# Kernel optimization log

Hardware: AMD Instinct MI355X
Metric: run time of the kernel (lower is better)

## Reference

```python
import jax, jax.numpy as jnp
import numpy as np
from functools import partial

N_FEATURES = 32
UNITS = [64, 32]
NUM_HEADS = 4
KEY_DIM = UNITS[-1] // NUM_HEADS  # 8
PRED_LEN = 24
B, T = 4096, 336


def _p(key, shape, scale=0.05):
    return scale * jax.random.normal(key, shape, dtype=jnp.float32)


def setup_inputs() -> dict:
    key = jax.random.key(0)
    ks = jax.random.split(key, 20)
    d = UNITS[-1]  # 32, model dim entering attention
    return {
        "x": jax.random.normal(ks[0], (B, T, N_FEATURES), dtype=jnp.float32),
        # LSTM layer 1: in=32, units=64
        "W1": _p(ks[1], (N_FEATURES, 4 * UNITS[0])),
        "U1": _p(ks[2], (UNITS[0], 4 * UNITS[0])),
        "b1": jnp.zeros((4 * UNITS[0],), jnp.float32),
        # LSTM layer 2: in=64, units=32
        "W2": _p(ks[3], (UNITS[0], 4 * UNITS[1])),
        "U2": _p(ks[4], (UNITS[1], 4 * UNITS[1])),
        "b2": jnp.zeros((4 * UNITS[1],), jnp.float32),
        # MultiHeadAttention projections (Keras layout)
        "Wq": _p(ks[5], (d, NUM_HEADS, KEY_DIM)),
        "bq": jnp.zeros((NUM_HEADS, KEY_DIM), jnp.float32),
        "Wk": _p(ks[6], (d, NUM_HEADS, KEY_DIM)),
        "bk": jnp.zeros((NUM_HEADS, KEY_DIM), jnp.float32),
        "Wv": _p(ks[7], (d, NUM_HEADS, KEY_DIM)),
        "bv": jnp.zeros((NUM_HEADS, KEY_DIM), jnp.float32),
        "Wo": _p(ks[8], (NUM_HEADS, KEY_DIM, d)),
        "bo": jnp.zeros((d,), jnp.float32),
        # Dense head
        "Wd1": _p(ks[9], (d, 64)),
        "bd1": jnp.zeros((64,), jnp.float32),
        "Wd2": _p(ks[10], (64, PRED_LEN)),
        "bd2": jnp.zeros((PRED_LEN,), jnp.float32),
    }


def _lstm(x, W, U, b, return_sequences):
    # x: [B, T, in]; Keras gate order: i, f, c(candidate), o
    Bb = x.shape[0]
    u = U.shape[0]
    x_t = jnp.swapaxes(x, 0, 1)  # [T, B, in]
    xz = x_t @ W + b             # precompute input contribution: [T, B, 4u]

    def step(carry, zx):
        h, c = carry
        z = zx + h @ U
        i, f, g, o = jnp.split(z, 4, axis=-1)
        i = jax.nn.sigmoid(i)
        f = jax.nn.sigmoid(f)
        g = jnp.tanh(g)
        o = jax.nn.sigmoid(o)
        c = f * c + i * g
        h = o * jnp.tanh(c)
        return (h, c), h

    init = (jnp.zeros((Bb, u), x.dtype), jnp.zeros((Bb, u), x.dtype))
    (h_last, _), hs = jax.lax.scan(step, init, xz)
    return jnp.swapaxes(hs, 0, 1) if return_sequences else h_last


def _mha_seq1(x, Wq, bq, Wk, bk, Wv, bv, Wo, bo):
    # x: [B, d]; attention over a seq-len-1 axis (faithful to tf.expand_dims)
    q = jnp.einsum('bd,dhk->bhk', x, Wq) + bq
    k = jnp.einsum('bd,dhk->bhk', x, Wk) + bk
    v = jnp.einsum('bd,dhk->bhk', x, Wv) + bv
    scores = jnp.sum(q * k, axis=-1, keepdims=True) / np.sqrt(KEY_DIM).astype(np.float32)  # [B,h,1]
    attn = jax.nn.softmax(scores, axis=-1)  # seq of 1 -> all ones, kept for fidelity
    o = attn * v  # [B,h,k]
    return jnp.einsum('bhk,hkd->bd', o, Wo) + bo


def reference(x, W1, U1, b1, W2, U2, b2, Wq, bq, Wk, bk, Wv, bv, Wo, bo, Wd1, bd1, Wd2, bd2):
    h = _lstm(x, W1, U1, b1, return_sequences=True)   # [B, T, 64]
    h = _lstm(h, W2, U2, b2, return_sequences=False)  # [B, 32]
    h = _mha_seq1(h, Wq, bq, Wk, bk, Wv, bv, Wo, bo)  # [B, 32]
    h = jax.nn.relu(h @ Wd1 + bd1)                    # [B, 64]
    return h @ Wd2 + bd2                              # [B, 24]
```

## Files before the change

### kernel.cpp

```cpp
#include <hip/hip_runtime.h>


#define B_TOTAL 4096
#define T_STEPS 336
#define NF      32
#define U1N     64
#define G1      256
#define U2N     32
#define G2      128
#define RROWS   8
#define NT      512
#define KH1     12
#define KG1     8
#define KH2     6
#define KG2     16

__device__ __forceinline__ float fast_sigmoid(float x) {
    return __fdividef(1.0f, 1.0f + __expf(-x));
}

__device__ __forceinline__ float fast_tanh(float x) {
    float ax = fabsf(x);
    float e  = __expf(-2.0f * ax);
    float r  = __fdividef(1.0f - e, 1.0f + e);
    return __builtin_copysignf(r, x);
}

__global__ __launch_bounds__(NT, 4) void lstm_fused(
    const float* __restrict__ x,
    const float* __restrict__ W1, const float* __restrict__ U1, const float* __restrict__ b1,
    const float* __restrict__ W2, const float* __restrict__ U2, const float* __restrict__ b2,
    const float* __restrict__ Wv, const float* __restrict__ bv,
    const float* __restrict__ Wo, const float* __restrict__ bo,
    const float* __restrict__ Wd1, const float* __restrict__ bd1,
    const float* __restrict__ Wd2, const float* __restrict__ bd2,
    float* __restrict__ out)
{
    __shared__ float act_sh[RROWS][128];
    __shared__ float zp[RROWS * KG1 * G1];

    const int tid = threadIdx.x;
    const int r0  = blockIdx.x * RROWS;

    const int ucol = tid & 63;
    const int kg1  = tid >> 6;
    const int u2   = tid & 31;
    const int kg2  = tid >> 5;
    const int g1r  = tid >> 6, g1u = tid & 63;
    const int g2r  = tid >> 5, g2u = tid & 31;

    float4 w1w[KH1];
    #pragma unroll
    for (int j = 0; j < KH1; ++j) {
        const int kk = KH1 * kg1 + j;
        const float* row = (kk < NF) ? (W1 + kk * G1) : (U1 + (kk - NF) * G1);
        w1w[j] = make_float4(row[ucol], row[64 + ucol], row[128 + ucol], row[192 + ucol]);
    }
    float4 b1v = make_float4(0.f, 0.f, 0.f, 0.f);
    if (kg1 == 0)
        b1v = make_float4(b1[ucol], b1[64 + ucol], b1[128 + ucol], b1[192 + ucol]);

    float4 w2w[KH2];
    #pragma unroll
    for (int j = 0; j < KH2; ++j) {
        const int kk = KH2 * kg2 + j;
        const float* row = (kk < U1N) ? (W2 + kk * G2) : (U2 + (kk - U1N) * G2);
        w2w[j] = make_float4(row[u2], row[32 + u2], row[64 + u2], row[96 + u2]);
    }
    float4 b2v = make_float4(0.f, 0.f, 0.f, 0.f);
    if (kg2 == 0)
        b2v = make_float4(b2[u2], b2[32 + u2], b2[64 + u2], b2[96 + u2]);

    reinterpret_cast<float2*>(&act_sh[0][0])[tid] = make_float2(0.f, 0.f);
    float c1 = 0.f, c2 = 0.f;

    const int xbase = (r0 + g2r) * (T_STEPS * NF) + g2u;
    __syncthreads();
    if (tid < 256) act_sh[g2r][g2u] = x[xbase];
    __syncthreads();

    for (int t = 0; t < T_STEPS; ++t) {
        float xnext = 0.f;
        if (tid < 256) {
            const int tn = (t + 1 < T_STEPS) ? (t + 1) : (T_STEPS - 1);
            xnext = x[xbase + tn * NF];
        }

        {
            const int ab = KH1 * kg1;
            #pragma unroll
            for (int r = 0; r < RROWS; ++r) {
                const float4* av = reinterpret_cast<const float4*>(&act_sh[r][ab]);
                const float4 a0 = av[0], a1 = av[1], a2 = av[2];
                float a[KH1];
                a[0]=a0.x; a[1]=a0.y; a[2]=a0.z;  a[3]=a0.w;
                a[4]=a1.x; a[5]=a1.y; a[6]=a1.z;  a[7]=a1.w;
                a[8]=a2.x; a[9]=a2.y; a[10]=a2.z; a[11]=a2.w;
                float4 acc = b1v;
                #pragma unroll
                for (int j = 0; j < KH1; ++j) {
                    acc.x = fmaf(a[j], w1w[j].x, acc.x);
                    acc.y = fmaf(a[j], w1w[j].y, acc.y);
                    acc.z = fmaf(a[j], w1w[j].z, acc.z);
                    acc.w = fmaf(a[j], w1w[j].w, acc.w);
                }
                *reinterpret_cast<float4*>(&zp[(r * KG1 + kg1) * G1 + 4 * ucol]) = acc;
            }
        }
        __syncthreads();

        {
            float4 z = make_float4(0.f, 0.f, 0.f, 0.f);
            #pragma unroll
            for (int k = 0; k < KG1; ++k) {
                const float4 p = *reinterpret_cast<const float4*>(&zp[(g1r * KG1 + k) * G1 + 4 * g1u]);
                z.x += p.x; z.y += p.y; z.z += p.z; z.w += p.w;
            }
            const float ig = fast_sigmoid(z.x);
            const float fg = fast_sigmoid(z.y);
            const float gg = fast_tanh(z.z);
            const float og = fast_sigmoid(z.w);
            c1 = fmaf(fg, c1, ig * gg);
            act_sh[g1r][NF + g1u] = og * fast_tanh(c1);
            if (tid < 256) act_sh[g2r][g2u] = xnext;
        }
        __syncthreads();

        {
            const int ab = NF + KH2 * kg2;
            #pragma unroll
            for (int r = 0; r < RROWS; ++r) {
                const float2* av = reinterpret_cast<const float2*>(&act_sh[r][ab]);
                const float2 a0 = av[0], a1 = av[1], a2 = av[2];
                float a[KH2];
                a[0]=a0.x; a[1]=a0.y; a[2]=a1.x; a[3]=a1.y; a[4]=a2.x; a[5]=a2.y;
                float4 acc = b2v;
                #pragma unroll
                for (int j = 0; j < KH2; ++j) {
                    acc.x = fmaf(a[j], w2w[j].x, acc.x);
                    acc.y = fmaf(a[j], w2w[j].y, acc.y);
                    acc.z = fmaf(a[j], w2w[j].z, acc.z);
                    acc.w = fmaf(a[j], w2w[j].w, acc.w);
                }
                *reinterpret_cast<float4*>(&zp[(r * KG2 + kg2) * G2 + 4 * u2]) = acc;
            }
        }
        __syncthreads();

        if (tid < 256) {
            float4 z = make_float4(0.f, 0.f, 0.f, 0.f);
            #pragma unroll
            for (int k = 0; k < KG2; ++k) {
                const float4 p = *reinterpret_cast<const float4*>(&zp[(g2r * KG2 + k) * G2 + 4 * g2u]);
                z.x += p.x; z.y += p.y; z.z += p.z; z.w += p.w;
            }
            const float ig = fast_sigmoid(z.x);
            const float fg = fast_sigmoid(z.y);
            const float gg = fast_tanh(z.z);
            const float og = fast_sigmoid(z.w);
            c2 = fmaf(fg, c2, ig * gg);
            act_sh[g2r][96 + g2u] = og * fast_tanh(c2);
        }
        __syncthreads();
    }

    {
        float* hb = &zp[0];
        if (tid < 256) {
            float acc = bv[g2u];
            #pragma unroll
            for (int j = 0; j < 32; ++j) acc = fmaf(act_sh[g2r][96 + j], Wv[j * 32 + g2u], acc);
            hb[tid] = acc;
        }
        __syncthreads();
        if (tid < 256) {
            float acc = bo[g2u];
            #pragma unroll
            for (int j = 0; j < 32; ++j) acc = fmaf(hb[g2r * 32 + j], Wo[j * 32 + g2u], acc);
            hb[256 + tid] = acc;
        }
        __syncthreads();
        {
            float acc = bd1[g1u];
            #pragma unroll
            for (int j = 0; j < 32; ++j) acc = fmaf(hb[256 + g1r * 32 + j], Wd1[j * 64 + g1u], acc);
            hb[512 + tid] = fmaxf(acc, 0.f);
        }
        __syncthreads();
        if (tid < RROWS * 24) {
            const int rr = tid / 24, cc = tid - rr * 24;
            float acc = bd2[cc];
            #pragma unroll
            for (int j = 0; j < 64; ++j) acc = fmaf(hb[512 + rr * 64 + j], Wd2[j * 24 + cc], acc);
            out[(r0 + rr) * 24 + cc] = acc;
        }
    }
}

extern "C" void kernel_launch(void* const* d_in, const int* in_sizes, int n_in,
                              void* d_out, int out_size, void* d_ws, size_t ws_size,
                              hipStream_t stream) {
    const float* x   = (const float*)d_in[0];
    const float* W1  = (const float*)d_in[1];
    const float* U1  = (const float*)d_in[2];
    const float* b1  = (const float*)d_in[3];
    const float* W2  = (const float*)d_in[4];
    const float* U2  = (const float*)d_in[5];
    const float* b2  = (const float*)d_in[6];
    const float* Wv  = (const float*)d_in[11];
    const float* bv  = (const float*)d_in[12];
    const float* Wo  = (const float*)d_in[13];
    const float* bo  = (const float*)d_in[14];
    const float* Wd1 = (const float*)d_in[15];
    const float* bd1 = (const float*)d_in[16];
    const float* Wd2 = (const float*)d_in[17];
    const float* bd2 = (const float*)d_in[18];
    float* outp = (float*)d_out;

    hipLaunchKernelGGL(lstm_fused, dim3(B_TOTAL / RROWS), dim3(NT), 0, stream,
                       x, W1, U1, b1, W2, U2, b2, Wv, bv, Wo, bo,
                       Wd1, bd1, Wd2, bd2, outp);
}
```

Before: 1.884 ms.

## Halve block size to 256 threads with two gate columns per thread

Drops the workgroup from 512 to 256 threads and has each thread compute two gate-column groups (A/B halves) for both LSTM layers, doubling its register-held weights. All threads now take part in the x prefetch, layer-2 cell update and head, so the tid<256 idle branches go away. The aim is cheaper per-step barriers and more work per thread, at the cost of more VGPRs and lower occupancy (launch bounds 2).

```diff
diff --git a/kernel.cpp b/kernel.cpp
--- a/kernel.cpp
+++ b/kernel.cpp
@@ -9,7 +9,7 @@
 #define U2N     32
 #define G2      128
 #define RROWS   8
-#define NT      512
+#define NT      256
 #define KH1     12
 #define KG1     8
 #define KH2     6
@@ -26,7 +26,7 @@
     return __builtin_copysignf(r, x);
 }
 
-__global__ __launch_bounds__(NT, 4) void lstm_fused(
+__global__ __launch_bounds__(NT, 2) void lstm_fused(
     const float* __restrict__ x,
     const float* __restrict__ W1, const float* __restrict__ U1, const float* __restrict__ b1,
     const float* __restrict__ W2, const float* __restrict__ U2, const float* __restrict__ b2,
@@ -42,49 +42,53 @@
     const int tid = threadIdx.x;
     const int r0  = blockIdx.x * RROWS;
 
-    const int ucol = tid & 63;
-    const int kg1  = tid >> 6;
-    const int u2   = tid & 31;
-    const int kg2  = tid >> 5;
-    const int g1r  = tid >> 6, g1u = tid & 63;
-    const int g2r  = tid >> 5, g2u = tid & 31;
-
-    float4 w1w[KH1];
+    const int kg1 = tid >> 5;
+    const int up1 = tid & 31;
+    const int kg2 = tid >> 4;
+    const int up2 = tid & 15;
+    const int pr  = tid >> 5, pu = tid & 31;
+
+    float4 w1a[KH1], w1b[KH1];
     #pragma unroll
     for (int j = 0; j < KH1; ++j) {
         const int kk = KH1 * kg1 + j;
         const float* row = (kk < NF) ? (W1 + kk * G1) : (U1 + (kk - NF) * G1);
-        w1w[j] = make_float4(row[ucol], row[64 + ucol], row[128 + ucol], row[192 + ucol]);
-    }
-    float4 b1v = make_float4(0.f, 0.f, 0.f, 0.f);
-    if (kg1 == 0)
-        b1v = make_float4(b1[ucol], b1[64 + ucol], b1[128 + ucol], b1[192 + ucol]);
-
-    float4 w2w[KH2];
+        w1a[j] = make_float4(row[up1],      row[64 + up1],  row[128 + up1], row[192 + up1]);
+        w1b[j] = make_float4(row[32 + up1], row[96 + up1],  row[160 + up1], row[224 + up1]);
+    }
+    float4 b1a = make_float4(0.f, 0.f, 0.f, 0.f);
+    float4 b1b = make_float4(0.f, 0.f, 0.f, 0.f);
+    if (kg1 == 0) {
+        b1a = make_float4(b1[up1],      b1[64 + up1], b1[128 + up1], b1[192 + up1]);
+        b1b = make_float4(b1[32 + up1], b1[96 + up1], b1[160 + up1], b1[224 + up1]);
+    }
+
+    float4 w2a[KH2], w2b[KH2];
     #pragma unroll
     for (int j = 0; j < KH2; ++j) {
         const int kk = KH2 * kg2 + j;
         const float* row = (kk < U1N) ? (W2 + kk * G2) : (U2 + (kk - U1N) * G2);
-        w2w[j] = make_float4(row[u2], row[32 + u2], row[64 + u2], row[96 + u2]);
-    }
-    float4 b2v = make_float4(0.f, 0.f, 0.f, 0.f);
-    if (kg2 == 0)
-        b2v = make_float4(b2[u2], b2[32 + u2], b2[64 + u2], b2[96 + u2]);
-
-    reinterpret_cast<float2*>(&act_sh[0][0])[tid] = make_float2(0.f, 0.f);
-    float c1 = 0.f, c2 = 0.f;
-
-    const int xbase = (r0 + g2r) * (T_STEPS * NF) + g2u;
+        w2a[j] = make_float4(row[up2],      row[32 + up2], row[64 + up2],  row[96 + up2]);
+        w2b[j] = make_float4(row[16 + up2], row[48 + up2], row[80 + up2],  row[112 + up2]);
+    }
+    float4 b2a = make_float4(0.f, 0.f, 0.f, 0.f);
+    float4 b2b = make_float4(0.f, 0.f, 0.f, 0.f);
+    if (kg2 == 0) {
+        b2a = make_float4(b2[up2],      b2[32 + up2], b2[64 + up2], b2[96 + up2]);
+        b2b = make_float4(b2[16 + up2], b2[48 + up2], b2[80 + up2], b2[112 + up2]);
+    }
+
+    reinterpret_cast<float4*>(&act_sh[0][0])[tid] = make_float4(0.f, 0.f, 0.f, 0.f);
+    float c1a = 0.f, c1b = 0.f, c2 = 0.f;
+
+    const int xbase = (r0 + pr) * (T_STEPS * NF) + pu;
     __syncthreads();
-    if (tid < 256) act_sh[g2r][g2u] = x[xbase];
+    act_sh[pr][pu] = x[xbase];
     __syncthreads();
 
     for (int t = 0; t < T_STEPS; ++t) {
-        float xnext = 0.f;
-        if (tid < 256) {
-            const int tn = (t + 1 < T_STEPS) ? (t + 1) : (T_STEPS - 1);
-            xnext = x[xbase + tn * NF];
-        }
+        const int tn = (t + 1 < T_STEPS) ? (t + 1) : (T_STEPS - 1);
+        const float xnext = x[xbase + tn * NF];
 
         {
             const int ab = KH1 * kg1;
@@ -96,62 +100,88 @@
                 a[0]=a0.x; a[1]=a0.y; a[2]=a0.z;  a[3]=a0.w;
                 a[4]=a1.x; a[5]=a1.y; a[6]=a1.z;  a[7]=a1.w;
                 a[8]=a2.x; a[9]=a2.y; a[10]=a2.z; a[11]=a2.w;
-                float4 acc = b1v;
+                float4 accA = b1a, accB = b1b;
                 #pragma unroll
                 for (int j = 0; j < KH1; ++j) {
-                    acc.x = fmaf(a[j], w1w[j].x, acc.x);
-                    acc.y = fmaf(a[j], w1w[j].y, acc.y);
-                    acc.z = fmaf(a[j], w1w[j].z, acc.z);
-                    acc.w = fmaf(a[j], w1w[j].w, acc.w);
+                    accA.x = fmaf(a[j], w1a[j].x, accA.x);
+                    accA.y = fmaf(a[j], w1a[j].y, accA.y);
+                    accA.z = fmaf(a[j], w1a[j].z, accA.z);
+                    accA.w = fmaf(a[j], w1a[j].w, accA.w);
+                    accB.x = fmaf(a[j], w1b[j].x, accB.x);
+                    accB.y = fmaf(a[j], w1b[j].y, accB.y);
+                    accB.z = fmaf(a[j], w1b[j].z, accB.z);
+                    accB.w = fmaf(a[j], w1b[j].w, accB.w);
                 }
-                *reinterpret_cast<float4*>(&zp[(r * KG1 + kg1) * G1 + 4 * ucol]) = acc;
-            }
-        }
-        __syncthreads();
-
-        {
-            float4 z = make_float4(0.f, 0.f, 0.f, 0.f);
+                float* zb = &zp[(r * KG1 + kg1) * G1];
+                *reinterpret_cast<float4*>(&zb[4 * up1])       = accA;
+                *reinterpret_cast<float4*>(&zb[128 + 4 * up1]) = accB;
+            }
+        }
+        __syncthreads();
+
+        {
+            float4 zA = make_float4(0.f, 0.f, 0.f, 0.f);
+            float4 zB = make_float4(0.f, 0.f, 0.f, 0.f);
             #pragma unroll
             for (int k = 0; k < KG1; ++k) {
-                const float4 p = *reinterpret_cast<const float4*>(&zp[(g1r * KG1 + k) * G1 + 4 * g1u]);
-                z.x += p.x; z.y += p.y; z.z += p.z; z.w += p.w;
-            }
-            const float ig = fast_sigmoid(z.x);
-            const float fg = fast_sigmoid(z.y);
-            const float gg = fast_tanh(z.z);
-            const float og = fast_sigmoid(z.w);
-            c1 = fmaf(fg, c1, ig * gg);
-            act_sh[g1r][NF + g1u] = og * fast_tanh(c1);
-            if (tid < 256) act_sh[g2r][g2u] = xnext;
-        }
-        __syncthreads();
-
-        {
-            const int ab = NF + KH2 * kg2;
+                const float* zb = &zp[(pr * KG1 + k) * G1];
+                const float4 pa = *reinterpret_cast<const float4*>(&zb[4 * pu]);
+                const float4 pb = *reinterpret_cast<const float4*>(&zb[128 + 4 * pu]);
+                zA.x += pa.x; zA.y += pa.y; zA.z += pa.z; zA.w += pa.w;
+                zB.x += pb.x; zB.y += pb.y; zB.z += pb.z; zB.w += pb.w;
+            }
+            {
+                const float ig = fast_sigmoid(zA.x);
+                const float fg = fast_sigmoid(zA.y);
+                const float gg = fast_tanh(zA.z);
+                const float og = fast_sigmoid(zA.w);
+                c1a = fmaf(fg, c1a, ig * gg);
+                act_sh[pr][NF + pu] = og * fast_tanh(c1a);
+            }
+            {
+                const float ig = fast_sigmoid(zB.x);
+                const float fg = fast_sigmoid(zB.y);
+                const float gg = fast_tanh(zB.z);
+                const float og = fast_sigmoid(zB.w);
+                c1b = fmaf(fg, c1b, ig * gg);
+                act_sh[pr][NF + 32 + pu] = og * fast_tanh(c1b);
+            }
+            act_sh[pr][pu] = xnext;
+        }
+        __syncthreads();
+
+        {
+            const int ab2 = NF + KH2 * kg2;
             #pragma unroll
             for (int r = 0; r < RROWS; ++r) {
-                const float2* av = reinterpret_cast<const float2*>(&act_sh[r][ab]);
+                const float2* av = reinterpret_cast<const float2*>(&act_sh[r][ab2]);
                 const float2 a0 = av[0], a1 = av[1], a2 = av[2];
                 float a[KH2];
                 a[0]=a0.x; a[1]=a0.y; a[2]=a1.x; a[3]=a1.y; a[4]=a2.x; a[5]=a2.y;
-                float4 acc = b2v;
+                float4 accA = b2a, accB = b2b;
                 #pragma unroll
                 for (int j = 0; j < KH2; ++j) {
-                    acc.x = fmaf(a[j], w2w[j].x, acc.x);
-                    acc.y = fmaf(a[j], w2w[j].y, acc.y);
-                    acc.z = fmaf(a[j], w2w[j].z, acc.z);
-                    acc.w = fmaf(a[j], w2w[j].w, acc.w);
+                    accA.x = fmaf(a[j], w2a[j].x, accA.x);
+                    accA.y = fmaf(a[j], w2a[j].y, accA.y);
+                    accA.z = fmaf(a[j], w2a[j].z, accA.z);
+                    accA.w = fmaf(a[j], w2a[j].w, accA.w);
+                    accB.x = fmaf(a[j], w2b[j].x, accB.x);
+                    accB.y = fmaf(a[j], w2b[j].y, accB.y);
+                    accB.z = fmaf(a[j], w2b[j].z, accB.z);
+                    accB.w = fmaf(a[j], w2b[j].w, accB.w);
                 }
-                *reinterpret_cast<float4*>(&zp[(r * KG2 + kg2) * G2 + 4 * u2]) = acc;
-            }
-        }
-        __syncthreads();
-
-        if (tid < 256) {
+                float* zb = &zp[(r * KG2 + kg2) * G2];
+                *reinterpret_cast<float4*>(&zb[4 * up2])      = accA;
+                *reinterpret_cast<float4*>(&zb[64 + 4 * up2]) = accB;
+            }
+        }
+        __syncthreads();
+
+        {
             float4 z = make_float4(0.f, 0.f, 0.f, 0.f);
             #pragma unroll
             for (int k = 0; k < KG2; ++k) {
-                const float4 p = *reinterpret_cast<const float4*>(&zp[(g2r * KG2 + k) * G2 + 4 * g2u]);
+                const float4 p = *reinterpret_cast<const float4*>(&zp[(pr * KG2 + k) * G2 + 4 * pu]);
                 z.x += p.x; z.y += p.y; z.z += p.z; z.w += p.w;
             }
             const float ig = fast_sigmoid(z.x);
@@ -159,32 +189,34 @@
             const float gg = fast_tanh(z.z);
             const float og = fast_sigmoid(z.w);
             c2 = fmaf(fg, c2, ig * gg);
-            act_sh[g2r][96 + g2u] = og * fast_tanh(c2);
+            act_sh[pr][96 + pu] = og * fast_tanh(c2);
         }
         __syncthreads();
     }
 
     {
         float* hb = &zp[0];
-        if (tid < 256) {
-            float acc = bv[g2u];
-            #pragma unroll
-            for (int j = 0; j < 32; ++j) acc = fmaf(act_sh[g2r][96 + j], Wv[j * 32 + g2u], acc);
+        {
+            float acc = bv[pu];
+            #pragma unroll
+            for (int j = 0; j < 32; ++j) acc = fmaf(act_sh[pr][96 + j], Wv[j * 32 + pu], acc);
             hb[tid] = acc;
         }
         __syncthreads();
-        if (tid < 256) {
-            float acc = bo[g2u];
-            #pragma unroll
-            for (int j = 0; j < 32; ++j) acc = fmaf(hb[g2r * 32 + j], Wo[j * 32 + g2u], acc);
+        {
+            float acc = bo[pu];
+            #pragma unroll
+            for (int j = 0; j < 32; ++j) acc = fmaf(hb[pr * 32 + j], Wo[j * 32 + pu], acc);
             hb[256 + tid] = acc;
         }
         __syncthreads();
-        {
-            float acc = bd1[g1u];
-            #pragma unroll
-            for (int j = 0; j < 32; ++j) acc = fmaf(hb[256 + g1r * 32 + j], Wd1[j * 64 + g1u], acc);
-            hb[512 + tid] = fmaxf(acc, 0.f);
+        #pragma unroll
+        for (int kk = 0; kk < 2; ++kk) {
+            const int c64 = pu + 32 * kk;
+            float acc = bd1[c64];
+            #pragma unroll
+            for (int j = 0; j < 32; ++j) acc = fmaf(hb[256 + pr * 32 + j], Wd1[j * 64 + c64], acc);
+            hb[512 + pr * 64 + c64] = fmaxf(acc, 0.f);
         }
         __syncthreads();
         if (tid < RROWS * 24) {
```

New measurement: 2.207 ms. 17.1% more time.

## Stage activations once per wavefront and broadcast them via readlane

Applied to the files above, without the earlier changes.

Each wavefront now does one float4 LDS load per lane, staging all 8 rows of its activation slice, and broadcasts the values with v_readlane instead of doing repeated per-row LDS reads. Layer 2 is repartitioned to match layer 1's 8 K-groups of 12 inputs, with each half-wave taking half the gates. This cuts the partial-sum reduction from 16 to 8 groups. The aim is to lower LDS read traffic and reduction work on the serial recurrence, at the cost of scalar readlane instructions and SGPR-to-VALU dependencies.

```diff
diff --git a/kernel.cpp b/kernel.cpp
--- a/kernel.cpp
+++ b/kernel.cpp
@@ -10,10 +10,8 @@
 #define G2      128
 #define RROWS   8
 #define NT      512
-#define KH1     12
 #define KG1     8
-#define KH2     6
-#define KG2     16
+#define APAD    132
 
 __device__ __forceinline__ float fast_sigmoid(float x) {
     return __fdividef(1.0f, 1.0f + __expf(-x));
@@ -24,6 +22,11 @@
     float e  = __expf(-2.0f * ax);
     float r  = __fdividef(1.0f - e, 1.0f + e);
     return __builtin_copysignf(r, x);
+}
+
+__device__ __forceinline__ float rl_get(const float4& stg, int c, int ln) {
+    const float v = (c == 0) ? stg.x : (c == 1) ? stg.y : (c == 2) ? stg.z : stg.w;
+    return __int_as_float(__builtin_amdgcn_readlane(__float_as_int(v), ln));
 }
 
 __global__ __launch_bounds__(NT, 4) void lstm_fused(
@@ -36,47 +39,53 @@
     const float* __restrict__ Wd2, const float* __restrict__ bd2,
     float* __restrict__ out)
 {
-    __shared__ float act_sh[RROWS][128];
+    __shared__ float act_sh[RROWS][APAD];
     __shared__ float zp[RROWS * KG1 * G1];
 
     const int tid = threadIdx.x;
     const int r0  = blockIdx.x * RROWS;
 
     const int ucol = tid & 63;
-    const int kg1  = tid >> 6;
+    const int wv   = tid >> 6;
+    const int sub  = (tid >> 5) & 1;
     const int u2   = tid & 31;
-    const int kg2  = tid >> 5;
     const int g1r  = tid >> 6, g1u = tid & 63;
-    const int g2r  = tid >> 5, g2u = tid & 31;
-
-    float4 w1w[KH1];
+    const int pr   = tid >> 5, pu = tid & 31;
+
+    float4 w1w[12];
     #pragma unroll
-    for (int j = 0; j < KH1; ++j) {
-        const int kk = KH1 * kg1 + j;
+    for (int j = 0; j < 12; ++j) {
+        const int kk = 12 * wv + j;
         const float* row = (kk < NF) ? (W1 + kk * G1) : (U1 + (kk - NF) * G1);
         w1w[j] = make_float4(row[ucol], row[64 + ucol], row[128 + ucol], row[192 + ucol]);
     }
     float4 b1v = make_float4(0.f, 0.f, 0.f, 0.f);
-    if (kg1 == 0)
+    if (wv == 0)
         b1v = make_float4(b1[ucol], b1[64 + ucol], b1[128 + ucol], b1[192 + ucol]);
 
-    float4 w2w[KH2];
+    float2 w2w[12];
     #pragma unroll
-    for (int j = 0; j < KH2; ++j) {
-        const int kk = KH2 * kg2 + j;
+    for (int j = 0; j < 12; ++j) {
+        const int kk = 12 * wv + j;
         const float* row = (kk < U1N) ? (W2 + kk * G2) : (U2 + (kk - U1N) * G2);
-        w2w[j] = make_float4(row[u2], row[32 + u2], row[64 + u2], row[96 + u2]);
-    }
-    float4 b2v = make_float4(0.f, 0.f, 0.f, 0.f);
-    if (kg2 == 0)
-        b2v = make_float4(b2[u2], b2[32 + u2], b2[64 + u2], b2[96 + u2]);
-
-    reinterpret_cast<float2*>(&act_sh[0][0])[tid] = make_float2(0.f, 0.f);
+        w2w[j] = make_float2(row[64 * sub + u2], row[64 * sub + 32 + u2]);
+    }
+    float2 b2p = make_float2(0.f, 0.f);
+    if (wv == 0)
+        b2p = make_float2(b2[64 * sub + u2], b2[64 * sub + 32 + u2]);
+
+    const int lane = tid & 63;
+    const int ch   = (lane < 24) ? lane : 23;
+    const int rc   = ch / 3, cc = ch % 3;
+    const float4* p1 = reinterpret_cast<const float4*>(&act_sh[rc][12 * wv + 4 * cc]);
+    const float4* p2 = reinterpret_cast<const float4*>(&act_sh[rc][NF + 12 * wv + 4 * cc]);
+
+    for (int i = tid; i < RROWS * APAD; i += NT) (&act_sh[0][0])[i] = 0.0f;
     float c1 = 0.f, c2 = 0.f;
 
-    const int xbase = (r0 + g2r) * (T_STEPS * NF) + g2u;
+    const int xbase = (r0 + pr) * (T_STEPS * NF) + pu;
     __syncthreads();
-    if (tid < 256) act_sh[g2r][g2u] = x[xbase];
+    if (tid < 256) act_sh[pr][pu] = x[xbase];
     __syncthreads();
 
     for (int t = 0; t < T_STEPS; ++t) {
@@ -87,24 +96,19 @@
         }
 
         {
-            const int ab = KH1 * kg1;
+            const float4 stg = *p1;
             #pragma unroll
             for (int r = 0; r < RROWS; ++r) {
-                const float4* av = reinterpret_cast<const float4*>(&act_sh[r][ab]);
-                const float4 a0 = av[0], a1 = av[1], a2 = av[2];
-                float a[KH1];
-                a[0]=a0.x; a[1]=a0.y; a[2]=a0.z;  a[3]=a0.w;
-                a[4]=a1.x; a[5]=a1.y; a[6]=a1.z;  a[7]=a1.w;
-                a[8]=a2.x; a[9]=a2.y; a[10]=a2.z; a[11]=a2.w;
                 float4 acc = b1v;
                 #pragma unroll
-                for (int j = 0; j < KH1; ++j) {
-                    acc.x = fmaf(a[j], w1w[j].x, acc.x);
-                    acc.y = fmaf(a[j], w1w[j].y, acc.y);
-                    acc.z = fmaf(a[j], w1w[j].z, acc.z);
-                    acc.w = fmaf(a[j], w1w[j].w, acc.w);
+                for (int j = 0; j < 12; ++j) {
+                    const float a = rl_get(stg, j & 3, 3 * r + (j >> 2));
+                    acc.x = fmaf(a, w1w[j].x, acc.x);
+                    acc.y = fmaf(a, w1w[j].y, acc.y);
+                    acc.z = fmaf(a, w1w[j].z, acc.z);
+                    acc.w = fmaf(a, w1w[j].w, acc.w);
                 }
-                *reinterpret_cast<float4*>(&zp[(r * KG1 + kg1) * G1 + 4 * ucol]) = acc;
+                *reinterpret_cast<float4*>(&zp[(r * KG1 + wv) * G1 + 4 * ucol]) = acc;
             }
         }
         __syncthreads();
@@ -122,27 +126,22 @@
             const float og = fast_sigmoid(z.w);
             c1 = fmaf(fg, c1, ig * gg);
             act_sh[g1r][NF + g1u] = og * fast_tanh(c1);
-            if (tid < 256) act_sh[g2r][g2u] = xnext;
-        }
-        __syncthreads();
-
-        {
-            const int ab = NF + KH2 * kg2;
+            if (tid < 256) act_sh[pr][pu] = xnext;
+        }
+        __syncthreads();
+
+        {
+            const float4 stg = *p2;
             #pragma unroll
             for (int r = 0; r < RROWS; ++r) {
-                const float2* av = reinterpret_cast<const float2*>(&act_sh[r][ab]);
-                const float2 a0 = av[0], a1 = av[1], a2 = av[2];
-                float a[KH2];
-                a[0]=a0.x; a[1]=a0.y; a[2]=a1.x; a[3]=a1.y; a[4]=a2.x; a[5]=a2.y;
-                float4 acc = b2v;
+                float2 acc = b2p;
                 #pragma unroll
-                for (int j = 0; j < KH2; ++j) {
-                    acc.x = fmaf(a[j], w2w[j].x, acc.x);
-                    acc.y = fmaf(a[j], w2w[j].y, acc.y);
-                    acc.z = fmaf(a[j], w2w[j].z, acc.z);
-                    acc.w = fmaf(a[j], w2w[j].w, acc.w);
+                for (int j = 0; j < 12; ++j) {
+                    const float a = rl_get(stg, j & 3, 3 * r + (j >> 2));
+                    acc.x = fmaf(a, w2w[j].x, acc.x);
+                    acc.y = fmaf(a, w2w[j].y, acc.y);
                 }
-                *reinterpret_cast<float4*>(&zp[(r * KG2 + kg2) * G2 + 4 * u2]) = acc;
+                *reinterpret_cast<float2*>(&zp[(r * 8 + wv) * G2 + 4 * u2 + 2 * sub]) = acc;
             }
         }
         __syncthreads();
@@ -150,8 +149,8 @@
         if (tid < 256) {
             float4 z = make_float4(0.f, 0.f, 0.f, 0.f);
             #pragma unroll
-            for (int k = 0; k < KG2; ++k) {
-                const float4 p = *reinterpret_cast<const float4*>(&zp[(g2r * KG2 + k) * G2 + 4 * g2u]);
+            for (int k = 0; k < 8; ++k) {
+                const float4 p = *reinterpret_cast<const float4*>(&zp[(pr * 8 + k) * G2 + 4 * pu]);
                 z.x += p.x; z.y += p.y; z.z += p.z; z.w += p.w;
             }
             const float ig = fast_sigmoid(z.x);
@@ -159,7 +158,7 @@
             const float gg = fast_tanh(z.z);
             const float og = fast_sigmoid(z.w);
             c2 = fmaf(fg, c2, ig * gg);
-            act_sh[g2r][96 + g2u] = og * fast_tanh(c2);
+            act_sh[pr][96 + pu] = og * fast_tanh(c2);
         }
         __syncthreads();
     }
@@ -167,16 +166,16 @@
     {
         float* hb = &zp[0];
         if (tid < 256) {
-            float acc = bv[g2u];
-            #pragma unroll
-            for (int j = 0; j < 32; ++j) acc = fmaf(act_sh[g2r][96 + j], Wv[j * 32 + g2u], acc);
+            float acc = bv[pu];
+            #pragma unroll
+            for (int j = 0; j < 32; ++j) acc = fmaf(act_sh[pr][96 + j], Wv[j * 32 + pu], acc);
             hb[tid] = acc;
         }
         __syncthreads();
         if (tid < 256) {
-            float acc = bo[g2u];
-            #pragma unroll
-            for (int j = 0; j < 32; ++j) acc = fmaf(hb[g2r * 32 + j], Wo[j * 32 + g2u], acc);
+            float acc = bo[pu];
+            #pragma unroll
+            for (int j = 0; j < 32; ++j) acc = fmaf(hb[pr * 32 + j], Wo[j * 32 + pu], acc);
             hb[256 + tid] = acc;
         }
         __syncthreads();
@@ -188,11 +187,11 @@
         }
         __syncthreads();
         if (tid < RROWS * 24) {
-            const int rr = tid / 24, cc = tid - rr * 24;
-            float acc = bd2[cc];
-            #pragma unroll
-            for (int j = 0; j < 64; ++j) acc = fmaf(hb[512 + rr * 64 + j], Wd2[j * 24 + cc], acc);
-            out[(r0 + rr) * 24 + cc] = acc;
+            const int rr = tid / 24, cci = tid - rr * 24;
+            float acc = bd2[cci];
+            #pragma unroll
+            for (int j = 0; j < 64; ++j) acc = fmaf(hb[512 + rr * 64 + j], Wd2[j * 24 + cci], acc);
+            out[(r0 + rr) * 24 + cci] = acc;
         }
     }
 }
```

Result: slower. 1.951 ms (+3.6%).
